# Optimization experiments

Hardware: AMD Instinct MI355X
Metric: run time of the kernel (lower is better)

The kernel has to match this reference:

```python
import jax, jax.numpy as jnp
import numpy as np

T, B, D, H, L = 512, 64, 512, 512, 2  # seq_len, batch, input, hidden, layers (bidirectional)


def _xavier(k, shape):
    fan_out, fan_in = shape
    lim = np.sqrt(6.0 / (fan_in + fan_out)).astype(np.float32)
    return jax.random.uniform(k, shape, minval=-lim, maxval=lim, dtype=jnp.float32)


def setup_inputs() -> dict:
    key = jax.random.key(0)
    ks = jax.random.split(key, 1 + 4 * L)
    inp = {"x": jax.random.normal(ks[0], (T, B, D), dtype=jnp.float32)}
    idx = 1
    for layer in range(L):
        din = D if layer == 0 else 2 * H
        for d in ("f", "b"):
            inp[f"w_ih{layer}_{d}"] = _xavier(ks[idx], (4 * H, din)); idx += 1
            inp[f"w_hh{layer}_{d}"] = _xavier(ks[idx], (4 * H, H)); idx += 1
            # xavier_uniform() in the module fills both biases with forget_bias=1.0
            inp[f"b_ih{layer}_{d}"] = jnp.ones((4 * H,), jnp.float32)
            inp[f"b_hh{layer}_{d}"] = jnp.ones((4 * H,), jnp.float32)
    return inp


def _lstm_dir(x, w_ih, w_hh, b_ih, b_hh, reverse):
    """Run one direction of a VarLSTMCell over time. x: [T,B,Din] -> h: [T,B,H]."""
    hdim = w_hh.shape[1]
    # precompute input contribution for all timesteps (same math as per-step matmul)
    xg = jnp.einsum('tbd,gd->tbg', x, w_ih) + b_ih + b_hh  # [T,B,4H]

    def step(carry, xg_t):
        h, c = carry
        gates = xg_t + h @ w_hh.T  # [B,4H]
        i, f, g, o = jnp.split(gates, 4, axis=-1)  # PyTorch LSTMCell gate order
        c = jax.nn.sigmoid(f) * c + jax.nn.sigmoid(i) * jnp.tanh(g)
        h = jax.nn.sigmoid(o) * jnp.tanh(c)
        return (h, c), h

    init = (jnp.zeros((x.shape[1], hdim), x.dtype), jnp.zeros((x.shape[1], hdim), x.dtype))
    _, hs = jax.lax.scan(step, init, xg, reverse=reverse)
    return hs  # [T,B,H], time-ordered (scan reverse keeps original ordering)


def reference(x,
              w_ih0_f, w_hh0_f, b_ih0_f, b_hh0_f,
              w_ih0_b, w_hh0_b, b_ih0_b, b_hh0_b,
              w_ih1_f, w_hh1_f, b_ih1_f, b_hh1_f,
              w_ih1_b, w_hh1_b, b_ih1_b, b_hh1_b):
    params = [
        ((w_ih0_f, w_hh0_f, b_ih0_f, b_hh0_f), (w_ih0_b, w_hh0_b, b_ih0_b, b_hh0_b)),
        ((w_ih1_f, w_hh1_f, b_ih1_f, b_hh1_f), (w_ih1_b, w_hh1_b, b_ih1_b, b_hh1_b)),
    ]
    out = x
    for fwd_p, bwd_p in params:
        h_f = _lstm_dir(out, *fwd_p, reverse=False)
        h_b = _lstm_dir(out, *bwd_p, reverse=True)
        out = jnp.concatenate([h_f, h_b], axis=-1)  # [T,B,2H]
        # dropout=0.0 -> inter-layer dropout is identity
    return out
```

## Files before the change

### kernel.cpp

```cpp
#include <hip/hip_runtime.h>
#include <hip/hip_bf16.h>
#include <stdint.h>


typedef __attribute__((ext_vector_type(8))) _Float16 half8;
typedef __attribute__((ext_vector_type(4))) float f32x4;
typedef __attribute__((ext_vector_type(4))) uint32_t u32x4;
typedef unsigned long long ull;

#define AS(p, v) __hip_atomic_store((p), (v), __ATOMIC_RELAXED, __HIP_MEMORY_SCOPE_AGENT)

#define TAGMASK 0x4000400040004000ULL
#define TM32    0x40004000u
#define PAT_L1A 0x0000400000004000ULL
#define PAT_L1B 0x4000000040000000ULL
#define PAT_INIT_LO 0x40004000u
#define PAT_INIT_HI 0x00000000u

__device__ __forceinline__ unsigned short f2h(float f) {
    union { _Float16 h; unsigned short u; } c; c.h = (_Float16)f; return c.u;
}
__device__ __forceinline__ float h2f(unsigned short u) {
    union { _Float16 h; unsigned short u; } c; c.u = u; return (float)c.h;
}

__global__ __launch_bounds__(256) void prep_kernel(
    const float* __restrict__ x,
    const float* __restrict__ w0f, const float* __restrict__ w0b,
    const float* __restrict__ w1f, const float* __restrict__ w1b,
    const float* __restrict__ bi0f, const float* __restrict__ bh0f,
    const float* __restrict__ bi0b, const float* __restrict__ bh0b,
    const float* __restrict__ bi1f, const float* __restrict__ bh1f,
    const float* __restrict__ bi1b, const float* __restrict__ bh1b,
    unsigned short* __restrict__ xh,
    unsigned short* __restrict__ wihh,
    float* __restrict__ bias,
    uint32_t* __restrict__ hbufi)
{
    const long total = 5801984L;
    long stride = (long)gridDim.x * blockDim.x;
    for (long i = (long)blockIdx.x * blockDim.x + threadIdx.x; i < total; i += stride) {
        if (i < 4194304L) {
            float4 v = ((const float4*)x)[i];
            ushort4 o; o.x=f2h(v.x); o.y=f2h(v.y); o.z=f2h(v.z); o.w=f2h(v.w);
            ((ushort4*)xh)[i] = o;
        } else if (i < 5767168L) {
            long j = i - 4194304L;
            const float* src; long sq;
            if (j < 262144L)       { src = w0f; sq = j;            }
            else if (j < 524288L)  { src = w0b; sq = j - 262144L;  }
            else if (j < 1048576L) { src = w1f; sq = j - 524288L;  }
            else                   { src = w1b; sq = j - 1048576L; }
            float4 v = ((const float4*)src)[sq];
            ushort4 o; o.x=f2h(v.x); o.y=f2h(v.y); o.z=f2h(v.z); o.w=f2h(v.w);
            ((ushort4*)wihh)[j] = o;
        } else if (i < 5769216L) {
            long j = i - 5767168L;
            int ld = (int)(j >> 9);
            long cq = j & 511L;
            const float* bi = ld==0?bi0f: ld==1?bi0b: ld==2?bi1f:bi1b;
            const float* bh = ld==0?bh0f: ld==1?bh0b: ld==2?bh1f:bh1b;
            float4 a = ((const float4*)bi)[cq];
            float4 b = ((const float4*)bh)[cq];
            float4 o; o.x=a.x+b.x; o.y=a.y+b.y; o.z=a.z+b.z; o.w=a.w+b.w;
            ((float4*)bias)[ld*512 + cq] = o;
        } else {
            long j = i - 5769216L;
            uint4 p; p.x=PAT_INIT_LO; p.y=PAT_INIT_HI; p.z=PAT_INIT_LO; p.w=PAT_INIT_HI;
            ((uint4*)hbufi)[j] = p;
        }
    }
}

__global__ __launch_bounds__(256) void gemm_xg(
    const unsigned short* __restrict__ A,
    const unsigned short* __restrict__ Wf,
    const unsigned short* __restrict__ Wb,
    unsigned short* __restrict__ xg,
    int Din)
{
    __shared__ __align__(16) unsigned short As[4096];
    __shared__ __align__(16) unsigned short Bs[4096];
    const int dir = blockIdx.z;
    const unsigned short* W = dir ? Wb : Wf;
    unsigned short* out = xg + (size_t)dir * 32768 * 2048;
    const int bn = blockIdx.x, bm = blockIdx.y;
    const int tid = threadIdx.x;
    const int wave = tid >> 6, lane = tid & 63;
    const int q = lane >> 4, ln = lane & 15;
    const int wm = wave >> 1, wn = wave & 1;

    f32x4 acc[4][4];
#pragma unroll
    for (int a = 0; a < 4; ++a)
#pragma unroll
        for (int b = 0; b < 4; ++b) acc[a][b] = (f32x4){0.f, 0.f, 0.f, 0.f};

    const int kiter = Din >> 5;
    for (int kb = 0; kb < kiter; ++kb) {
        __syncthreads();
#pragma unroll
        for (int i = 0; i < 2; ++i) {
            int off = i*4096 + wave*1024 + lane*16;
            int row = off >> 6;
            int kel = (off & 63) >> 1;
            const unsigned short* sa = A + (size_t)(bm*128 + row)*Din + kb*32 + kel;
            const unsigned short* sb = W + (size_t)(bn*128 + row)*Din + kb*32 + kel;
            __builtin_amdgcn_global_load_lds(
                (const __attribute__((address_space(1))) uint32_t*)sa,
                (__attribute__((address_space(3))) uint32_t*)((char*)As + i*4096 + wave*1024),
                16, 0, 0);
            __builtin_amdgcn_global_load_lds(
                (const __attribute__((address_space(1))) uint32_t*)sb,
                (__attribute__((address_space(3))) uint32_t*)((char*)Bs + i*4096 + wave*1024),
                16, 0, 0);
        }
        __syncthreads();
        half8 af[4], bf[4];
#pragma unroll
        for (int mt = 0; mt < 4; ++mt)
            af[mt] = *(const half8*)((const char*)As + (wm*64 + mt*16 + ln)*64 + q*16);
#pragma unroll
        for (int nt = 0; nt < 4; ++nt)
            bf[nt] = *(const half8*)((const char*)Bs + (wn*64 + nt*16 + ln)*64 + q*16);
#pragma unroll
        for (int mt = 0; mt < 4; ++mt)
#pragma unroll
            for (int nt = 0; nt < 4; ++nt)
                acc[mt][nt] = __builtin_amdgcn_mfma_f32_16x16x32_f16(af[mt], bf[nt], acc[mt][nt], 0, 0, 0);
    }
    const int tt = bm*2 + wm;
#pragma unroll
    for (int mt = 0; mt < 4; ++mt)
#pragma unroll
        for (int nt = 0; nt < 4; ++nt) {
            int col = bn*128 + wn*64 + nt*16 + ln;
            int gate = col >> 9, colg = col & 511;
            union { unsigned short u[4]; ull v; } p;
#pragma unroll
            for (int r = 0; r < 4; ++r) p.u[r] = f2h(acc[mt][nt][r]);
            __builtin_nontemporal_store(p.v,
                (ull*)(out + (((size_t)tt*4 + gate)*512 + colg)*64 + mt*16 + q*4));
        }
}

__global__ __launch_bounds__(512, 2) void rec_kernel(
    const unsigned short* __restrict__ xg,
    const float* __restrict__ whhf,
    const float* __restrict__ whhb,
    const float* __restrict__ bias,
    unsigned short* __restrict__ hbuf,
    unsigned short* __restrict__ outh,
    float* __restrict__ outf,
    const int layer)
{
    __shared__ __align__(16) unsigned short h_lds[8192];
    __shared__ __align__(16) float accbuf[2048];
    __shared__ __align__(16) unsigned short htile[512];

    const int bx = blockIdx.x;
    const int dir = bx & 1, bh = (bx >> 1) & 3, cg = bx >> 3;
    const int R0 = bh * 16, C0 = cg * 32;
    const int tid = threadIdx.x;
    const int wv = tid >> 6, lane = tid & 63;
    const int g = wv >> 1, wc = wv & 1;
    const int ln = lane & 15, q = lane >> 4;
    const float* whhg = dir ? whhb : whhf;

    const ull pat0 = layer ? PAT_L1A : 0ULL;
    const ull pat1 = layer ? PAT_L1B : TAGMASK;
    const uint32_t ep0 = (uint32_t)(pat0 & 0xffffffffULL);
    const uint32_t ep1 = (uint32_t)(pat1 & 0xffffffffULL);

    half8 wreg[16];
    {
        const int wrow = g*512 + C0 + wc*16 + ln;
        const float* wsrc = whhg + (size_t)wrow * 512 + q*8;
#pragma unroll
        for (int kk = 0; kk < 16; ++kk) {
            float4 v0 = *(const float4*)(wsrc + kk*32);
            float4 v1 = *(const float4*)(wsrc + kk*32 + 4);
            union { unsigned short u[8]; half8 v; } p;
            p.u[0]=f2h(v0.x); p.u[1]=f2h(v0.y); p.u[2]=f2h(v0.z); p.u[3]=f2h(v0.w);
            p.u[4]=f2h(v1.x); p.u[5]=f2h(v1.y); p.u[6]=f2h(v1.z); p.u[7]=f2h(v1.w);
            wreg[kk] = p.v;
        }
    }

    const unsigned short* xgd = xg + (size_t)dir * 32768 * 2048;
    const float* biasd = bias + dir * 2048;
    const int myc = C0 + wc*16 + ln;
    float bv0 = biasd[0*512 + myc];
    float bv1 = biasd[1*512 + myc];
    float bv2 = biasd[2*512 + myc];
    float bv3 = biasd[3*512 + myc];
    float carr[4] = {0.f, 0.f, 0.f, 0.f};

    const int prow = tid >> 5;
    const int pcol = (tid & 31) * 16;
    const int swz  = (prow & 7) << 4;
    const int wb0 = prow*1024 + ((pcol*2)      ^ swz);
    const int wb1 = prow*1024 + ((pcol*2 + 16) ^ swz);

#pragma unroll 1
    for (int s = 0; s < 512; ++s) {
        const int t = dir ? (511 - s) : s;

        ull xv64[4] = {0,0,0,0};
        if (g == 0) {
#pragma unroll
            for (int nt_ = 0; nt_ < 4; ++nt_)
                xv64[nt_] = __builtin_nontemporal_load(
                    (const ull*)(xgd + ((size_t)(t*4 + nt_)*512 + myc)*64 + bh*16 + q*4));
        }

        if (s > 0) {
            const int slot_r = (s - 1) & 3;
            const uint32_t ep = (((s - 1) >> 2) & 1) ? ep1 : ep0;
            const uint32_t* src = (const uint32_t*)(hbuf
                + ((size_t)(slot_r*2 + dir)*64 + R0 + prow)*512 + pcol);
            u32x4 r0, r1;
            bool ok = false;
            for (int it = 0; it < (1 << 13) && !ok; ++it) {
                asm volatile(
                    "global_load_dwordx4 %0, %2, off sc0 sc1\n\t"
                    "global_load_dwordx4 %1, %3, off sc0 sc1\n\t"
                    "s_waitcnt vmcnt(0)"
                    : "=&v"(r0), "=&v"(r1)
                    : "v"(src), "v"(src + 4)
                    : "memory");
                uint32_t bad = 0;
#pragma unroll
                for (int c = 0; c < 4; ++c) bad |= (r0[c] ^ ep) & TM32;
#pragma unroll
                for (int c = 0; c < 4; ++c) bad |= (r1[c] ^ ep) & TM32;
                ok = (bad == 0);
            }
#pragma unroll
            for (int c = 0; c < 4; ++c) { r0[c] &= ~TM32; r1[c] &= ~TM32; }
            *(u32x4*)((char*)h_lds + wb0) = r0;
            *(u32x4*)((char*)h_lds + wb1) = r1;
        }
        __syncthreads();

        f32x4 acc = (f32x4){0.f, 0.f, 0.f, 0.f};
        if (s > 0) {
            const char* hbase = (const char*)h_lds + ln*1024;
            const int lswz = (ln & 7) << 4;
#pragma unroll
            for (int kk = 0; kk < 16; ++kk) {
                half8 a = *(const half8*)(hbase + ((kk*64 + q*16) ^ lswz));
                acc = __builtin_amdgcn_mfma_f32_16x16x32_f16(a, wreg[kk], acc, 0, 0, 0);
            }
        }
        *(f32x4*)&accbuf[(wv*16 + ln)*16 + q*4] = acc;
        __syncthreads();

        if (g == 0) {
            f32x4 a0 = *(const f32x4*)&accbuf[((0*2 + wc)*16 + ln)*16 + q*4];
            f32x4 a1 = *(const f32x4*)&accbuf[((1*2 + wc)*16 + ln)*16 + q*4];
            f32x4 a2 = *(const f32x4*)&accbuf[((2*2 + wc)*16 + ln)*16 + q*4];
            f32x4 a3 = *(const f32x4*)&accbuf[((3*2 + wc)*16 + ln)*16 + q*4];
            unsigned short hs[4];
#pragma unroll
            for (int r = 0; r < 4; ++r) {
                float gi = a0[r] + h2f((unsigned short)(xv64[0] >> (16*r))) + bv0;
                float gf = a1[r] + h2f((unsigned short)(xv64[1] >> (16*r))) + bv1;
                float gg = a2[r] + h2f((unsigned short)(xv64[2] >> (16*r))) + bv2;
                float go = a3[r] + h2f((unsigned short)(xv64[3] >> (16*r))) + bv3;
                float si = 1.f / (1.f + __expf(-gi));
                float sf = 1.f / (1.f + __expf(-gf));
                float so = 1.f / (1.f + __expf(-go));
                float tg = 2.f / (1.f + __expf(-2.f*gg)) - 1.f;
                float c  = sf * carr[r] + si * tg;
                carr[r] = c;
                float th = 2.f / (1.f + __expf(-2.f*c)) - 1.f;
                hs[r] = f2h(so * th);
            }
            unsigned short* ht = htile + wc*256;
#pragma unroll
            for (int r = 0; r < 4; ++r) ht[(q*4 + r)*16 + ln] = hs[r];
            ull hv64 = *(const ull*)(ht + (lane >> 2)*16 + (lane & 3)*4);
            const int row  = R0 + (lane >> 2);
            const int colw = C0 + wc*16 + (lane & 3)*4;

            const int slot_w = s & 3;
            const ull wpat = ((s >> 2) & 1) ? pat1 : pat0;
            AS((ull*)(hbuf + ((size_t)(slot_w*2 + dir)*64 + row)*512 + colw), hv64 | wpat);

            if (layer == 0) {
                __builtin_nontemporal_store(hv64,
                    (ull*)(outh + ((size_t)t*64 + row)*1024 + dir*512 + colw));
            } else {
                union { ull u; unsigned short us[4]; } pu; pu.u = hv64;
                union { ull u; float f[2]; } o0, o1;
                o0.f[0] = h2f(pu.us[0]); o0.f[1] = h2f(pu.us[1]);
                o1.f[0] = h2f(pu.us[2]); o1.f[1] = h2f(pu.us[3]);
                ull* dst = (ull*)(outf + ((size_t)t*64 + row)*1024 + dir*512 + colw);
                __builtin_nontemporal_store(o0.u, dst);
                __builtin_nontemporal_store(o1.u, dst + 1);
            }
        }
    }
}

extern "C" void kernel_launch(void* const* d_in, const int* in_sizes, int n_in,
                              void* d_out, int out_size, void* d_ws, size_t ws_size,
                              hipStream_t stream)
{
    (void)in_sizes; (void)n_in; (void)out_size; (void)ws_size;
    const float* x       = (const float*)d_in[0];
    const float* w_ih0_f = (const float*)d_in[1];
    const float* w_hh0_f = (const float*)d_in[2];
    const float* b_ih0_f = (const float*)d_in[3];
    const float* b_hh0_f = (const float*)d_in[4];
    const float* w_ih0_b = (const float*)d_in[5];
    const float* w_hh0_b = (const float*)d_in[6];
    const float* b_ih0_b = (const float*)d_in[7];
    const float* b_hh0_b = (const float*)d_in[8];
    const float* w_ih1_f = (const float*)d_in[9];
    const float* w_hh1_f = (const float*)d_in[10];
    const float* b_ih1_f = (const float*)d_in[11];
    const float* b_hh1_f = (const float*)d_in[12];
    const float* w_ih1_b = (const float*)d_in[13];
    const float* w_hh1_b = (const float*)d_in[14];
    const float* b_ih1_b = (const float*)d_in[15];
    const float* b_hh1_b = (const float*)d_in[16];

    char* ws = (char*)d_ws;
    unsigned short* xg    = (unsigned short*)(ws + 0);
    unsigned short* wihh  = (unsigned short*)(ws + 268435456L);
    float*          bias  = (float*)         (ws + 281018368L);
    unsigned short* hbuf  = (unsigned short*)(ws + 281051136L);

    unsigned short* in1 = (unsigned short*)d_out;
    unsigned short* xh  = (unsigned short*)((char*)d_out + 67108864L);
    float* outf = (float*)d_out;

    prep_kernel<<<dim3(1024), dim3(256), 0, stream>>>(
        x, w_ih0_f, w_ih0_b, w_ih1_f, w_ih1_b,
        b_ih0_f, b_hh0_f, b_ih0_b, b_hh0_b,
        b_ih1_f, b_hh1_f, b_ih1_b, b_hh1_b,
        xh, wihh, bias, (uint32_t*)hbuf);

    gemm_xg<<<dim3(16, 256, 2), dim3(256), 0, stream>>>(
        xh, wihh, wihh + 1048576, xg, 512);
    rec_kernel<<<dim3(128), dim3(512), 0, stream>>>(
        xg, w_hh0_f, w_hh0_b, bias, hbuf, in1, (float*)nullptr, 0);

    gemm_xg<<<dim3(16, 256, 2), dim3(256), 0, stream>>>(
        in1, wihh + 2097152, wihh + 4194304, xg, 1024);
    rec_kernel<<<dim3(128), dim3(512), 0, stream>>>(
        xg, w_hh1_f, w_hh1_b, bias + 4096, hbuf,
        (unsigned short*)nullptr, outf, 1);
}
```

Measured before the change: 5.589 ms.

## Interleave forward and backward directions in one block of the recurrent kernel

Each recurrent block now handles both directions for its tile, alternating forward and backward half-steps, with double-buffered LDS and both weight sets held in registers. The grid is halved from 128 to 64 blocks. The aim is to hide cross-block flag-poll latency for one direction behind the other direction's compute, and to prefetch the next step's input gates a step ahead. In exchange it doubles register pressure for weights and serialises two directions per block, which may reduce parallelism and occupancy.

```diff
diff --git a/kernel.cpp b/kernel.cpp
--- a/kernel.cpp
+++ b/kernel.cpp
@@ -144,6 +144,112 @@
         }
 }
 
+struct RecCtx {
+    const unsigned short* hbuf_c;
+    unsigned short* hbuf;
+    unsigned short* outh;
+    float* outf;
+    int layer, R0, C0, tid, wv, lane, g, wc, ln, q;
+    int c0row, colq, wb0, wb1;
+    uint32_t ep0, ep1;
+    ull pat0, pat1;
+};
+
+__device__ __forceinline__ void poll_stage(const RecCtx& cx, int d, int sm1,
+                                           unsigned short* lbuf)
+{
+    const int slot_r = sm1 & 3;
+    const uint32_t ep = ((sm1 >> 2) & 1) ? cx.ep1 : cx.ep0;
+    const uint32_t* s0 = (const uint32_t*)(cx.hbuf_c
+        + ((size_t)(slot_r*2 + d)*64 + cx.R0 + cx.c0row)*512 + cx.colq);
+    const uint32_t* s1 = (const uint32_t*)(cx.hbuf_c
+        + ((size_t)(slot_r*2 + d)*64 + cx.R0 + cx.c0row + 8)*512 + cx.colq);
+    u32x4 r0, r1;
+    bool ok = false;
+    for (int it = 0; it < (1 << 13) && !ok; ++it) {
+        asm volatile(
+            "global_load_dwordx4 %0, %2, off sc0 sc1\n\t"
+            "global_load_dwordx4 %1, %3, off sc0 sc1\n\t"
+            "s_waitcnt vmcnt(0)"
+            : "=&v"(r0), "=&v"(r1)
+            : "v"(s0), "v"(s1)
+            : "memory");
+        uint32_t bad = 0;
+#pragma unroll
+        for (int c = 0; c < 4; ++c) bad |= (r0[c] ^ ep) & TM32;
+#pragma unroll
+        for (int c = 0; c < 4; ++c) bad |= (r1[c] ^ ep) & TM32;
+        ok = (bad == 0);
+    }
+#pragma unroll
+    for (int c = 0; c < 4; ++c) { r0[c] &= ~TM32; r1[c] &= ~TM32; }
+    *(u32x4*)((char*)lbuf + cx.wb0) = r0;
+    *(u32x4*)((char*)lbuf + cx.wb1) = r1;
+}
+
+__device__ __forceinline__ void mfma_phase(const RecCtx& cx,
+    const unsigned short* lbuf, const half8* wreg, float* achb)
+{
+    f32x4 acc = (f32x4){0.f, 0.f, 0.f, 0.f};
+    const char* hbase = (const char*)lbuf + cx.ln*1024;
+    const int lswz = (cx.ln & 7) << 4;
+#pragma unroll
+    for (int kk = 0; kk < 16; ++kk) {
+        half8 a = *(const half8*)(hbase + ((kk*64 + cx.q*16) ^ lswz));
+        acc = __builtin_amdgcn_mfma_f32_16x16x32_f16(a, wreg[kk], acc, 0, 0, 0);
+    }
+    *(f32x4*)&achb[(cx.wv*16 + cx.ln)*20 + cx.q*4] = acc;
+}
+
+__device__ __forceinline__ void pointwise(const RecCtx& cx, int d, int s, int t,
+    const ull* xv, float* carr, const float* achb, unsigned short* htb,
+    float bv0, float bv1, float bv2, float bv3)
+{
+    f32x4 a0 = *(const f32x4*)&achb[((0*2 + cx.wc)*16 + cx.ln)*20 + cx.q*4];
+    f32x4 a1 = *(const f32x4*)&achb[((1*2 + cx.wc)*16 + cx.ln)*20 + cx.q*4];
+    f32x4 a2 = *(const f32x4*)&achb[((2*2 + cx.wc)*16 + cx.ln)*20 + cx.q*4];
+    f32x4 a3 = *(const f32x4*)&achb[((3*2 + cx.wc)*16 + cx.ln)*20 + cx.q*4];
+    unsigned short hs[4];
+#pragma unroll
+    for (int r = 0; r < 4; ++r) {
+        float gi = a0[r] + h2f((unsigned short)(xv[0] >> (16*r))) + bv0;
+        float gf = a1[r] + h2f((unsigned short)(xv[1] >> (16*r))) + bv1;
+        float gg = a2[r] + h2f((unsigned short)(xv[2] >> (16*r))) + bv2;
+        float go = a3[r] + h2f((unsigned short)(xv[3] >> (16*r))) + bv3;
+        float si = 1.f / (1.f + __expf(-gi));
+        float sf = 1.f / (1.f + __expf(-gf));
+        float so = 1.f / (1.f + __expf(-go));
+        float tg = 2.f / (1.f + __expf(-2.f*gg)) - 1.f;
+        float c  = sf * carr[r] + si * tg;
+        carr[r] = c;
+        float th = 2.f / (1.f + __expf(-2.f*c)) - 1.f;
+        hs[r] = f2h(so * th);
+    }
+    unsigned short* ht = htb + cx.wc*256;
+#pragma unroll
+    for (int r = 0; r < 4; ++r) ht[(cx.q*4 + r)*16 + cx.ln] = hs[r];
+    ull hv64 = *(const ull*)(ht + (cx.lane >> 2)*16 + (cx.lane & 3)*4);
+    const int row  = cx.R0 + (cx.lane >> 2);
+    const int colw = cx.C0 + cx.wc*16 + (cx.lane & 3)*4;
+
+    const int slot_w = s & 3;
+    const ull wpat = ((s >> 2) & 1) ? cx.pat1 : cx.pat0;
+    AS((ull*)(cx.hbuf + ((size_t)(slot_w*2 + d)*64 + row)*512 + colw), hv64 | wpat);
+
+    if (cx.layer == 0) {
+        __builtin_nontemporal_store(hv64,
+            (ull*)(cx.outh + ((size_t)t*64 + row)*1024 + d*512 + colw));
+    } else {
+        union { ull u; unsigned short us[4]; } pu; pu.u = hv64;
+        union { ull u; float f[2]; } o0, o1;
+        o0.f[0] = h2f(pu.us[0]); o0.f[1] = h2f(pu.us[1]);
+        o1.f[0] = h2f(pu.us[2]); o1.f[1] = h2f(pu.us[3]);
+        ull* dst = (ull*)(cx.outf + ((size_t)t*64 + row)*1024 + d*512 + colw);
+        __builtin_nontemporal_store(o0.u, dst);
+        __builtin_nontemporal_store(o1.u, dst + 1);
+    }
+}
+
 __global__ __launch_bounds__(512, 2) void rec_kernel(
     const unsigned short* __restrict__ xg,
     const float* __restrict__ whhf,
@@ -154,152 +260,120 @@
     float* __restrict__ outf,
     const int layer)
 {
-    __shared__ __align__(16) unsigned short h_lds[8192];
-    __shared__ __align__(16) float accbuf[2048];
-    __shared__ __align__(16) unsigned short htile[512];
+    __shared__ __align__(16) unsigned short h_lds[2][8192];
+    __shared__ __align__(16) float accbuf[2][2560];
+    __shared__ __align__(16) unsigned short htile[2][512];
 
     const int bx = blockIdx.x;
-    const int dir = bx & 1, bh = (bx >> 1) & 3, cg = bx >> 3;
-    const int R0 = bh * 16, C0 = cg * 32;
-    const int tid = threadIdx.x;
-    const int wv = tid >> 6, lane = tid & 63;
-    const int g = wv >> 1, wc = wv & 1;
-    const int ln = lane & 15, q = lane >> 4;
-    const float* whhg = dir ? whhb : whhf;
-
-    const ull pat0 = layer ? PAT_L1A : 0ULL;
-    const ull pat1 = layer ? PAT_L1B : TAGMASK;
-    const uint32_t ep0 = (uint32_t)(pat0 & 0xffffffffULL);
-    const uint32_t ep1 = (uint32_t)(pat1 & 0xffffffffULL);
-
-    half8 wreg[16];
+    RecCtx cx;
+    cx.hbuf_c = hbuf; cx.hbuf = hbuf; cx.outh = outh; cx.outf = outf;
+    cx.layer = layer;
+    const int bh = bx & 3, cg = bx >> 2;
+    cx.R0 = bh * 16; cx.C0 = cg * 32;
+    cx.tid = threadIdx.x;
+    cx.wv = cx.tid >> 6; cx.lane = cx.tid & 63;
+    cx.g = cx.wv >> 1; cx.wc = cx.wv & 1;
+    cx.ln = cx.lane & 15; cx.q = cx.lane >> 4;
+    cx.pat0 = layer ? PAT_L1A : 0ULL;
+    cx.pat1 = layer ? PAT_L1B : TAGMASK;
+    cx.ep0 = (uint32_t)(cx.pat0 & 0xffffffffULL);
+    cx.ep1 = (uint32_t)(cx.pat1 & 0xffffffffULL);
+    cx.c0row = cx.tid >> 6;
+    cx.colq  = (cx.tid & 63) * 8;
+    cx.wb0 = cx.c0row*1024 + (((cx.tid & 63)*16) ^ ((cx.c0row & 7) << 4));
+    cx.wb1 = (cx.c0row + 8)*1024 + (((cx.tid & 63)*16) ^ ((cx.c0row & 7) << 4));
+
+    half8 wregA[16], wregB[16];
     {
-        const int wrow = g*512 + C0 + wc*16 + ln;
-        const float* wsrc = whhg + (size_t)wrow * 512 + q*8;
+        const int wrow = cx.g*512 + cx.C0 + cx.wc*16 + cx.ln;
+        const float* srcA = whhf + (size_t)wrow * 512 + cx.q*8;
+        const float* srcB = whhb + (size_t)wrow * 512 + cx.q*8;
 #pragma unroll
         for (int kk = 0; kk < 16; ++kk) {
-            float4 v0 = *(const float4*)(wsrc + kk*32);
-            float4 v1 = *(const float4*)(wsrc + kk*32 + 4);
+            float4 v0 = *(const float4*)(srcA + kk*32);
+            float4 v1 = *(const float4*)(srcA + kk*32 + 4);
             union { unsigned short u[8]; half8 v; } p;
             p.u[0]=f2h(v0.x); p.u[1]=f2h(v0.y); p.u[2]=f2h(v0.z); p.u[3]=f2h(v0.w);
             p.u[4]=f2h(v1.x); p.u[5]=f2h(v1.y); p.u[6]=f2h(v1.z); p.u[7]=f2h(v1.w);
-            wreg[kk] = p.v;
-        }
-    }
-
-    const unsigned short* xgd = xg + (size_t)dir * 32768 * 2048;
-    const float* biasd = bias + dir * 2048;
-    const int myc = C0 + wc*16 + ln;
-    float bv0 = biasd[0*512 + myc];
-    float bv1 = biasd[1*512 + myc];
-    float bv2 = biasd[2*512 + myc];
-    float bv3 = biasd[3*512 + myc];
-    float carr[4] = {0.f, 0.f, 0.f, 0.f};
-
-    const int prow = tid >> 5;
-    const int pcol = (tid & 31) * 16;
-    const int swz  = (prow & 7) << 4;
-    const int wb0 = prow*1024 + ((pcol*2)      ^ swz);
-    const int wb1 = prow*1024 + ((pcol*2 + 16) ^ swz);
+            wregA[kk] = p.v;
+        }
+#pragma unroll
+        for (int kk = 0; kk < 16; ++kk) {
+            float4 v0 = *(const float4*)(srcB + kk*32);
+            float4 v1 = *(const float4*)(srcB + kk*32 + 4);
+            union { unsigned short u[8]; half8 v; } p;
+            p.u[0]=f2h(v0.x); p.u[1]=f2h(v0.y); p.u[2]=f2h(v0.z); p.u[3]=f2h(v0.w);
+            p.u[4]=f2h(v1.x); p.u[5]=f2h(v1.y); p.u[6]=f2h(v1.z); p.u[7]=f2h(v1.w);
+            wregB[kk] = p.v;
+        }
+    }
+
+    const unsigned short* xgdA = xg;
+    const unsigned short* xgdB = xg + (size_t)32768 * 2048;
+    const int myc = cx.C0 + cx.wc*16 + cx.ln;
+    float bvA0 = bias[0*512 + myc],        bvA1 = bias[1*512 + myc];
+    float bvA2 = bias[2*512 + myc],        bvA3 = bias[3*512 + myc];
+    float bvB0 = bias[2048 + 0*512 + myc], bvB1 = bias[2048 + 1*512 + myc];
+    float bvB2 = bias[2048 + 2*512 + myc], bvB3 = bias[2048 + 3*512 + myc];
+    float carrA[4] = {0.f,0.f,0.f,0.f}, carrB[4] = {0.f,0.f,0.f,0.f};
+    ull xvA[4] = {0,0,0,0}, xvB[4] = {0,0,0,0};
+    ull xvAn[4] = {0,0,0,0}, xvBn[4] = {0,0,0,0};
+
+    const size_t xoff = (size_t)bh*16 + cx.q*4;
+
+    {
+        f32x4 z = (f32x4){0.f,0.f,0.f,0.f};
+        *(f32x4*)&accbuf[0][(cx.wv*16 + cx.ln)*20 + cx.q*4] = z;
+        *(f32x4*)&accbuf[1][(cx.wv*16 + cx.ln)*20 + cx.q*4] = z;
+        __syncthreads();
+        if (cx.g == 0) {
+#pragma unroll
+            for (int k = 0; k < 4; ++k) {
+                xvA[k] = __builtin_nontemporal_load(
+                    (const ull*)(xgdA + ((size_t)(0*4 + k)*512 + myc)*64 + xoff));
+                xvB[k] = __builtin_nontemporal_load(
+                    (const ull*)(xgdB + ((size_t)(511*4 + k)*512 + myc)*64 + xoff));
+            }
+            pointwise(cx, 0, 0, 0,   xvA, carrA, accbuf[0], htile[0], bvA0,bvA1,bvA2,bvA3);
+            pointwise(cx, 1, 0, 511, xvB, carrB, accbuf[1], htile[1], bvB0,bvB1,bvB2,bvB3);
+#pragma unroll
+            for (int k = 0; k < 4; ++k) {
+                xvA[k] = __builtin_nontemporal_load(
+                    (const ull*)(xgdA + ((size_t)(1*4 + k)*512 + myc)*64 + xoff));
+                xvB[k] = __builtin_nontemporal_load(
+                    (const ull*)(xgdB + ((size_t)(510*4 + k)*512 + myc)*64 + xoff));
+            }
+        }
+    }
 
 #pragma unroll 1
-    for (int s = 0; s < 512; ++s) {
-        const int t = dir ? (511 - s) : s;
-
-        ull xv64[4] = {0,0,0,0};
-        if (g == 0) {
-#pragma unroll
-            for (int nt_ = 0; nt_ < 4; ++nt_)
-                xv64[nt_] = __builtin_nontemporal_load(
-                    (const ull*)(xgd + ((size_t)(t*4 + nt_)*512 + myc)*64 + bh*16 + q*4));
-        }
-
-        if (s > 0) {
-            const int slot_r = (s - 1) & 3;
-            const uint32_t ep = (((s - 1) >> 2) & 1) ? ep1 : ep0;
-            const uint32_t* src = (const uint32_t*)(hbuf
-                + ((size_t)(slot_r*2 + dir)*64 + R0 + prow)*512 + pcol);
-            u32x4 r0, r1;
-            bool ok = false;
-            for (int it = 0; it < (1 << 13) && !ok; ++it) {
-                asm volatile(
-                    "global_load_dwordx4 %0, %2, off sc0 sc1\n\t"
-                    "global_load_dwordx4 %1, %3, off sc0 sc1\n\t"
-                    "s_waitcnt vmcnt(0)"
-                    : "=&v"(r0), "=&v"(r1)
-                    : "v"(src), "v"(src + 4)
-                    : "memory");
-                uint32_t bad = 0;
-#pragma unroll
-                for (int c = 0; c < 4; ++c) bad |= (r0[c] ^ ep) & TM32;
-#pragma unroll
-                for (int c = 0; c < 4; ++c) bad |= (r1[c] ^ ep) & TM32;
-                ok = (bad == 0);
+    for (int s = 1; s < 512; ++s) {
+        const int tA = s, tB = 511 - s;
+
+        poll_stage(cx, 0, s - 1, h_lds[0]);
+        __syncthreads();
+        if (cx.g == 0 && s < 511) {
+#pragma unroll
+            for (int k = 0; k < 4; ++k) {
+                xvAn[k] = __builtin_nontemporal_load(
+                    (const ull*)(xgdA + ((size_t)((s+1)*4 + k)*512 + myc)*64 + xoff));
+                xvBn[k] = __builtin_nontemporal_load(
+                    (const ull*)(xgdB + ((size_t)((510-s)*4 + k)*512 + myc)*64 + xoff));
             }
-#pragma unroll
-            for (int c = 0; c < 4; ++c) { r0[c] &= ~TM32; r1[c] &= ~TM32; }
-            *(u32x4*)((char*)h_lds + wb0) = r0;
-            *(u32x4*)((char*)h_lds + wb1) = r1;
-        }
-        __syncthreads();
-
-        f32x4 acc = (f32x4){0.f, 0.f, 0.f, 0.f};
-        if (s > 0) {
-            const char* hbase = (const char*)h_lds + ln*1024;
-            const int lswz = (ln & 7) << 4;
-#pragma unroll
-            for (int kk = 0; kk < 16; ++kk) {
-                half8 a = *(const half8*)(hbase + ((kk*64 + q*16) ^ lswz));
-                acc = __builtin_amdgcn_mfma_f32_16x16x32_f16(a, wreg[kk], acc, 0, 0, 0);
-            }
-        }
-        *(f32x4*)&accbuf[(wv*16 + ln)*16 + q*4] = acc;
-        __syncthreads();
-
-        if (g == 0) {
-            f32x4 a0 = *(const f32x4*)&accbuf[((0*2 + wc)*16 + ln)*16 + q*4];
-            f32x4 a1 = *(const f32x4*)&accbuf[((1*2 + wc)*16 + ln)*16 + q*4];
-            f32x4 a2 = *(const f32x4*)&accbuf[((2*2 + wc)*16 + ln)*16 + q*4];
-            f32x4 a3 = *(const f32x4*)&accbuf[((3*2 + wc)*16 + ln)*16 + q*4];
-            unsigned short hs[4];
-#pragma unroll
-            for (int r = 0; r < 4; ++r) {
-                float gi = a0[r] + h2f((unsigned short)(xv64[0] >> (16*r))) + bv0;
-                float gf = a1[r] + h2f((unsigned short)(xv64[1] >> (16*r))) + bv1;
-                float gg = a2[r] + h2f((unsigned short)(xv64[2] >> (16*r))) + bv2;
-                float go = a3[r] + h2f((unsigned short)(xv64[3] >> (16*r))) + bv3;
-                float si = 1.f / (1.f + __expf(-gi));
-                float sf = 1.f / (1.f + __expf(-gf));
-                float so = 1.f / (1.f + __expf(-go));
-                float tg = 2.f / (1.f + __expf(-2.f*gg)) - 1.f;
-                float c  = sf * carr[r] + si * tg;
-                carr[r] = c;
-                float th = 2.f / (1.f + __expf(-2.f*c)) - 1.f;
-                hs[r] = f2h(so * th);
-            }
-            unsigned short* ht = htile + wc*256;
-#pragma unroll
-            for (int r = 0; r < 4; ++r) ht[(q*4 + r)*16 + ln] = hs[r];
-            ull hv64 = *(const ull*)(ht + (lane >> 2)*16 + (lane & 3)*4);
-            const int row  = R0 + (lane >> 2);
-            const int colw = C0 + wc*16 + (lane & 3)*4;
-
-            const int slot_w = s & 3;
-            const ull wpat = ((s >> 2) & 1) ? pat1 : pat0;
-            AS((ull*)(hbuf + ((size_t)(slot_w*2 + dir)*64 + row)*512 + colw), hv64 | wpat);
-
-            if (layer == 0) {
-                __builtin_nontemporal_store(hv64,
-                    (ull*)(outh + ((size_t)t*64 + row)*1024 + dir*512 + colw));
-            } else {
-                union { ull u; unsigned short us[4]; } pu; pu.u = hv64;
-                union { ull u; float f[2]; } o0, o1;
-                o0.f[0] = h2f(pu.us[0]); o0.f[1] = h2f(pu.us[1]);
-                o1.f[0] = h2f(pu.us[2]); o1.f[1] = h2f(pu.us[3]);
-                ull* dst = (ull*)(outf + ((size_t)t*64 + row)*1024 + dir*512 + colw);
-                __builtin_nontemporal_store(o0.u, dst);
-                __builtin_nontemporal_store(o1.u, dst + 1);
-            }
+        }
+        mfma_phase(cx, h_lds[0], wregA, accbuf[0]);
+        __syncthreads();
+        if (cx.g == 0)
+            pointwise(cx, 0, s, tA, xvA, carrA, accbuf[0], htile[0], bvA0,bvA1,bvA2,bvA3);
+
+        poll_stage(cx, 1, s - 1, h_lds[1]);
+        __syncthreads();
+        mfma_phase(cx, h_lds[1], wregB, accbuf[1]);
+        __syncthreads();
+        if (cx.g == 0) {
+            pointwise(cx, 1, s, tB, xvB, carrB, accbuf[1], htile[1], bvB0,bvB1,bvB2,bvB3);
+#pragma unroll
+            for (int k = 0; k < 4; ++k) { xvA[k] = xvAn[k]; xvB[k] = xvBn[k]; }
         }
     }
 }
@@ -345,12 +419,12 @@
 
     gemm_xg<<<dim3(16, 256, 2), dim3(256), 0, stream>>>(
         xh, wihh, wihh + 1048576, xg, 512);
-    rec_kernel<<<dim3(128), dim3(512), 0, stream>>>(
+    rec_kernel<<<dim3(64), dim3(512), 0, stream>>>(
         xg, w_hh0_f, w_hh0_b, bias, hbuf, in1, (float*)nullptr, 0);
 
     gemm_xg<<<dim3(16, 256, 2), dim3(256), 0, stream>>>(
         in1, wihh + 2097152, wihh + 4194304, xg, 1024);
-    rec_kernel<<<dim3(128), dim3(512), 0, stream>>>(
+    rec_kernel<<<dim3(64), dim3(512), 0, stream>>>(
         xg, w_hh1_f, w_hh1_b, bias + 4096, hbuf,
         (unsigned short*)nullptr, outf, 1);
 }
```

New measurement: 5.106 ms. 1.09x faster.

## Interleave both LSTM directions per block with pipelined hidden-state loads

Applied to the files above, without the earlier changes.

Each recurrent block now handles both the forward and backward directions for its row and column tile, keeping both recurrent weight sets in registers and halving the grid to 64 blocks. The hidden-state ring reads for one direction are issued while the other direction does its MFMA and pointwise work, so polling latency overlaps with compute. Gates are laid out so one wave holds all four gates of a column and combines them with lane shuffles, which drops the shared-memory accumulator exchange and one barrier. Register pressure doubles (launch bounds drop to one block per CU) and each step is now serialized over two directions within a block.

```diff
diff --git a/kernel.cpp b/kernel.cpp
--- a/kernel.cpp
+++ b/kernel.cpp
@@ -144,7 +144,7 @@
         }
 }
 
-__global__ __launch_bounds__(512, 2) void rec_kernel(
+__global__ __launch_bounds__(512, 1) void rec_kernel(
     const unsigned short* __restrict__ xg,
     const float* __restrict__ whhf,
     const float* __restrict__ whhb,
@@ -154,153 +154,199 @@
     float* __restrict__ outf,
     const int layer)
 {
-    __shared__ __align__(16) unsigned short h_lds[8192];
-    __shared__ __align__(16) float accbuf[2048];
+    __shared__ __align__(16) unsigned short h_lds[32768];
     __shared__ __align__(16) unsigned short htile[512];
 
     const int bx = blockIdx.x;
-    const int dir = bx & 1, bh = (bx >> 1) & 3, cg = bx >> 3;
-    const int R0 = bh * 16, C0 = cg * 32;
+    const int bh = bx & 3, cg = bx >> 2;
+    const int R0 = bh*16, C0 = cg*32;
     const int tid = threadIdx.x;
     const int wv = tid >> 6, lane = tid & 63;
-    const int g = wv >> 1, wc = wv & 1;
     const int ln = lane & 15, q = lane >> 4;
-    const float* whhg = dir ? whhb : whhf;
+    const int gate = ln & 3, lc = ln >> 2;
+    const int col = C0 + wv*4 + lc;
 
     const ull pat0 = layer ? PAT_L1A : 0ULL;
     const ull pat1 = layer ? PAT_L1B : TAGMASK;
     const uint32_t ep0 = (uint32_t)(pat0 & 0xffffffffULL);
     const uint32_t ep1 = (uint32_t)(pat1 & 0xffffffffULL);
-
-    half8 wreg[16];
+    const uint32_t NC = layer ? 0u : 0x40000000u;
+
+    half8 wregA[16], wregB[16];
     {
-        const int wrow = g*512 + C0 + wc*16 + ln;
-        const float* wsrc = whhg + (size_t)wrow * 512 + q*8;
+        const float* srcA = whhf + (size_t)(gate*512 + col)*512 + q*8;
+        const float* srcB = whhb + (size_t)(gate*512 + col)*512 + q*8;
 #pragma unroll
         for (int kk = 0; kk < 16; ++kk) {
-            float4 v0 = *(const float4*)(wsrc + kk*32);
-            float4 v1 = *(const float4*)(wsrc + kk*32 + 4);
+            float4 v0 = *(const float4*)(srcA + kk*32);
+            float4 v1 = *(const float4*)(srcA + kk*32 + 4);
             union { unsigned short u[8]; half8 v; } p;
             p.u[0]=f2h(v0.x); p.u[1]=f2h(v0.y); p.u[2]=f2h(v0.z); p.u[3]=f2h(v0.w);
             p.u[4]=f2h(v1.x); p.u[5]=f2h(v1.y); p.u[6]=f2h(v1.z); p.u[7]=f2h(v1.w);
-            wreg[kk] = p.v;
+            wregA[kk] = p.v;
+        }
+#pragma unroll
+        for (int kk = 0; kk < 16; ++kk) {
+            float4 v0 = *(const float4*)(srcB + kk*32);
+            float4 v1 = *(const float4*)(srcB + kk*32 + 4);
+            union { unsigned short u[8]; half8 v; } p;
+            p.u[0]=f2h(v0.x); p.u[1]=f2h(v0.y); p.u[2]=f2h(v0.z); p.u[3]=f2h(v0.w);
+            p.u[4]=f2h(v1.x); p.u[5]=f2h(v1.y); p.u[6]=f2h(v1.z); p.u[7]=f2h(v1.w);
+            wregB[kk] = p.v;
         }
     }
 
-    const unsigned short* xgd = xg + (size_t)dir * 32768 * 2048;
-    const float* biasd = bias + dir * 2048;
-    const int myc = C0 + wc*16 + ln;
-    float bv0 = biasd[0*512 + myc];
-    float bv1 = biasd[1*512 + myc];
-    float bv2 = biasd[2*512 + myc];
-    float bv3 = biasd[3*512 + myc];
-    float carr[4] = {0.f, 0.f, 0.f, 0.f};
-
-    const int prow = tid >> 5;
-    const int pcol = (tid & 31) * 16;
-    const int swz  = (prow & 7) << 4;
-    const int wb0 = prow*1024 + ((pcol*2)      ^ swz);
-    const int wb1 = prow*1024 + ((pcol*2 + 16) ^ swz);
-
-#pragma unroll 1
-    for (int s = 0; s < 512; ++s) {
-        const int t = dir ? (511 - s) : s;
-
-        ull xv64[4] = {0,0,0,0};
-        if (g == 0) {
-#pragma unroll
-            for (int nt_ = 0; nt_ < 4; ++nt_)
-                xv64[nt_] = __builtin_nontemporal_load(
-                    (const ull*)(xgd + ((size_t)(t*4 + nt_)*512 + myc)*64 + bh*16 + q*4));
-        }
-
-        if (s > 0) {
-            const int slot_r = (s - 1) & 3;
-            const uint32_t ep = (((s - 1) >> 2) & 1) ? ep1 : ep0;
-            const uint32_t* src = (const uint32_t*)(hbuf
-                + ((size_t)(slot_r*2 + dir)*64 + R0 + prow)*512 + pcol);
-            u32x4 r0, r1;
-            bool ok = false;
-            for (int it = 0; it < (1 << 13) && !ok; ++it) {
-                asm volatile(
-                    "global_load_dwordx4 %0, %2, off sc0 sc1\n\t"
-                    "global_load_dwordx4 %1, %3, off sc0 sc1\n\t"
-                    "s_waitcnt vmcnt(0)"
-                    : "=&v"(r0), "=&v"(r1)
-                    : "v"(src), "v"(src + 4)
-                    : "memory");
-                uint32_t bad = 0;
-#pragma unroll
-                for (int c = 0; c < 4; ++c) bad |= (r0[c] ^ ep) & TM32;
-#pragma unroll
-                for (int c = 0; c < 4; ++c) bad |= (r1[c] ^ ep) & TM32;
-                ok = (bad == 0);
+    const int c0row = tid >> 6;
+    const int colq  = (tid & 63) * 8;
+    const int swz   = (c0row & 7) << 4;
+    const int wb0 = c0row*1024 + (((tid & 63)*16) ^ swz);
+    const int wb1 = (c0row + 8)*1024 + (((tid & 63)*16) ^ swz);
+
+    const unsigned short* xgdA = xg;
+    const unsigned short* xgdB = xg + (size_t)32768 * 2048;
+    const float bvA = bias[gate*512 + col];
+    const float bvB = bias[2048 + gate*512 + col];
+    float carrA[4] = {0.f,0.f,0.f,0.f}, carrB[4] = {0.f,0.f,0.f,0.f};
+
+    auto xga = [&](int t) { return (const ull*)(xgdA + ((size_t)(t*4 + gate)*512 + col)*64 + bh*16 + q*4); };
+    auto xgb = [&](int t) { return (const ull*)(xgdB + ((size_t)(t*4 + gate)*512 + col)*64 + bh*16 + q*4); };
+    auto ringaddr = [&](int d, int sm1) {
+        return (const uint32_t*)(hbuf + ((size_t)((sm1 & 3)*2 + d)*64 + R0 + c0row)*512 + colq);
+    };
+
+    auto TAGS = [&](const u32x4& r0, const u32x4& r1, uint32_t ep) -> uint32_t {
+        uint32_t bad = 0;
+#pragma unroll
+        for (int c = 0; c < 4; ++c) bad |= (r0[c] ^ ep) & TM32;
+#pragma unroll
+        for (int c = 0; c < 4; ++c) bad |= (r1[c] ^ ep) & TM32;
+        return bad;
+    };
+    auto ISSUE = [&](u32x4& r0, u32x4& r1, const uint32_t* a0) {
+        r0 = (u32x4){NC, NC, NC, NC};
+        r1 = (u32x4){NC, NC, NC, NC};
+        asm volatile("global_load_dwordx4 %0, %2, off sc0 sc1\n\t"
+                     "global_load_dwordx4 %1, %3, off sc0 sc1"
+                     : "+v"(r0), "+v"(r1)
+                     : "v"(a0), "v"(a0 + 2048) : "memory");
+    };
+    auto CHECKSTAGE = [&](u32x4& r0, u32x4& r1, const uint32_t* a0, uint32_t ep,
+                          unsigned short* lbuf, int N) {
+        if (N == 2) asm volatile("s_waitcnt vmcnt(2)" : "+v"(r0), "+v"(r1) :: "memory");
+        else        asm volatile("s_waitcnt vmcnt(4)" : "+v"(r0), "+v"(r1) :: "memory");
+        uint32_t bad = TAGS(r0, r1, ep);
+        if (__builtin_expect(bad != 0, 0)) {
+            asm volatile("s_waitcnt vmcnt(0)" : "+v"(r0), "+v"(r1) :: "memory");
+            bad = TAGS(r0, r1, ep);
+            for (int it = 0; bad && it < (1 << 13); ++it) {
+                asm volatile("global_load_dwordx4 %0, %2, off sc0 sc1\n\t"
+                             "global_load_dwordx4 %1, %3, off sc0 sc1\n\t"
+                             "s_waitcnt vmcnt(0)"
+                             : "+v"(r0), "+v"(r1)
+                             : "v"(a0), "v"(a0 + 2048) : "memory");
+                bad = TAGS(r0, r1, ep);
             }
-#pragma unroll
-            for (int c = 0; c < 4; ++c) { r0[c] &= ~TM32; r1[c] &= ~TM32; }
-            *(u32x4*)((char*)h_lds + wb0) = r0;
-            *(u32x4*)((char*)h_lds + wb1) = r1;
-        }
-        __syncthreads();
-
-        f32x4 acc = (f32x4){0.f, 0.f, 0.f, 0.f};
-        if (s > 0) {
-            const char* hbase = (const char*)h_lds + ln*1024;
-            const int lswz = (ln & 7) << 4;
-#pragma unroll
-            for (int kk = 0; kk < 16; ++kk) {
-                half8 a = *(const half8*)(hbase + ((kk*64 + q*16) ^ lswz));
-                acc = __builtin_amdgcn_mfma_f32_16x16x32_f16(a, wreg[kk], acc, 0, 0, 0);
-            }
-        }
-        *(f32x4*)&accbuf[(wv*16 + ln)*16 + q*4] = acc;
-        __syncthreads();
-
-        if (g == 0) {
-            f32x4 a0 = *(const f32x4*)&accbuf[((0*2 + wc)*16 + ln)*16 + q*4];
-            f32x4 a1 = *(const f32x4*)&accbuf[((1*2 + wc)*16 + ln)*16 + q*4];
-            f32x4 a2 = *(const f32x4*)&accbuf[((2*2 + wc)*16 + ln)*16 + q*4];
-            f32x4 a3 = *(const f32x4*)&accbuf[((3*2 + wc)*16 + ln)*16 + q*4];
-            unsigned short hs[4];
-#pragma unroll
-            for (int r = 0; r < 4; ++r) {
-                float gi = a0[r] + h2f((unsigned short)(xv64[0] >> (16*r))) + bv0;
-                float gf = a1[r] + h2f((unsigned short)(xv64[1] >> (16*r))) + bv1;
-                float gg = a2[r] + h2f((unsigned short)(xv64[2] >> (16*r))) + bv2;
-                float go = a3[r] + h2f((unsigned short)(xv64[3] >> (16*r))) + bv3;
-                float si = 1.f / (1.f + __expf(-gi));
-                float sf = 1.f / (1.f + __expf(-gf));
-                float so = 1.f / (1.f + __expf(-go));
-                float tg = 2.f / (1.f + __expf(-2.f*gg)) - 1.f;
-                float c  = sf * carr[r] + si * tg;
-                carr[r] = c;
-                float th = 2.f / (1.f + __expf(-2.f*c)) - 1.f;
-                hs[r] = f2h(so * th);
-            }
-            unsigned short* ht = htile + wc*256;
-#pragma unroll
-            for (int r = 0; r < 4; ++r) ht[(q*4 + r)*16 + ln] = hs[r];
-            ull hv64 = *(const ull*)(ht + (lane >> 2)*16 + (lane & 3)*4);
-            const int row  = R0 + (lane >> 2);
-            const int colw = C0 + wc*16 + (lane & 3)*4;
-
-            const int slot_w = s & 3;
+        }
+        u32x4 w0 = r0, w1 = r1;
+#pragma unroll
+        for (int c = 0; c < 4; ++c) { w0[c] &= ~TM32; w1[c] &= ~TM32; }
+        *(u32x4*)((char*)lbuf + wb0) = w0;
+        *(u32x4*)((char*)lbuf + wb1) = w1;
+    };
+    auto MFMA = [&](const unsigned short* lbuf, const half8* wreg) -> f32x4 {
+        f32x4 acc = (f32x4){0.f,0.f,0.f,0.f};
+        const char* hb = (const char*)lbuf + ln*1024;
+        const int lswz = (ln & 7) << 4;
+#pragma unroll
+        for (int kk = 0; kk < 16; ++kk) {
+            half8 a = *(const half8*)(hb + ((kk*64 + q*16) ^ lswz));
+            acc = __builtin_amdgcn_mfma_f32_16x16x32_f16(a, wreg[kk], acc, 0, 0, 0);
+        }
+        return acc;
+    };
+    auto PW = [&](int d, int s, int t, f32x4 acc, ull xv, float* carr, float bv) {
+        unsigned short hs[4];
+#pragma unroll
+        for (int r = 0; r < 4; ++r) {
+            float v  = acc[r] + h2f((unsigned short)(xv >> (16*r))) + bv;
+            float o1 = __shfl_xor(v, 1);
+            float e  = (gate & 1) ? o1 : v;
+            float od = (gate & 1) ? v  : o1;
+            float e2 = __shfl_xor(e, 2);
+            float od2= __shfl_xor(od, 2);
+            float gi = (gate & 2) ? e2 : e;
+            float gg = (gate & 2) ? e  : e2;
+            float gf = (gate & 2) ? od2: od;
+            float go = (gate & 2) ? od : od2;
+            float si = 1.f / (1.f + __expf(-gi));
+            float sf = 1.f / (1.f + __expf(-gf));
+            float so = 1.f / (1.f + __expf(-go));
+            float tg = 2.f / (1.f + __expf(-2.f*gg)) - 1.f;
+            float c  = sf * carr[r] + si * tg;
+            carr[r] = c;
+            float th = 2.f / (1.f + __expf(-2.f*c)) - 1.f;
+            hs[r] = f2h(so * th);
+        }
+        if (gate == 0) {
+#pragma unroll
+            for (int r = 0; r < 4; ++r) htile[wv*64 + (q*4 + r)*4 + lc] = hs[r];
+        }
+        if (lane < 16) {
+            ull hv64 = *(const ull*)(htile + wv*64 + lane*4);
+            const int row  = R0 + lane;
+            const int colb = C0 + wv*4;
             const ull wpat = ((s >> 2) & 1) ? pat1 : pat0;
-            AS((ull*)(hbuf + ((size_t)(slot_w*2 + dir)*64 + row)*512 + colw), hv64 | wpat);
-
+            AS((ull*)(hbuf + ((size_t)((s & 3)*2 + d)*64 + row)*512 + colb), hv64 | wpat);
             if (layer == 0) {
                 __builtin_nontemporal_store(hv64,
-                    (ull*)(outh + ((size_t)t*64 + row)*1024 + dir*512 + colw));
+                    (ull*)(outh + ((size_t)t*64 + row)*1024 + d*512 + colb));
             } else {
                 union { ull u; unsigned short us[4]; } pu; pu.u = hv64;
-                union { ull u; float f[2]; } o0, o1;
-                o0.f[0] = h2f(pu.us[0]); o0.f[1] = h2f(pu.us[1]);
-                o1.f[0] = h2f(pu.us[2]); o1.f[1] = h2f(pu.us[3]);
-                ull* dst = (ull*)(outf + ((size_t)t*64 + row)*1024 + dir*512 + colw);
-                __builtin_nontemporal_store(o0.u, dst);
-                __builtin_nontemporal_store(o1.u, dst + 1);
+                f32x4 o; o[0]=h2f(pu.us[0]); o[1]=h2f(pu.us[1]);
+                o[2]=h2f(pu.us[2]); o[3]=h2f(pu.us[3]);
+                __builtin_nontemporal_store(o,
+                    (f32x4*)(outf + ((size_t)t*64 + row)*1024 + d*512 + colb));
             }
         }
+    };
+
+    u32x4 rA0, rA1, rB0, rB1;
+    ull xvA, xvB, xvAn, xvBn;
+
+    {
+        f32x4 z = (f32x4){0.f,0.f,0.f,0.f};
+        xvA = __builtin_nontemporal_load(xga(0));
+        xvB = __builtin_nontemporal_load(xgb(511));
+        PW(0, 0, 0,   z, xvA, carrA, bvA);
+        PW(1, 0, 511, z, xvB, carrB, bvB);
+        xvA = __builtin_nontemporal_load(xga(1));
+        xvB = __builtin_nontemporal_load(xgb(510));
+        ISSUE(rA0, rA1, ringaddr(0, 0));
+    }
+
+#pragma unroll 1
+    for (int s = 1; s < 512; ++s) {
+        const int tA = s, tB = 511 - s;
+        unsigned short* bufA = h_lds + ((s & 1)) * 8192;
+        unsigned short* bufB = h_lds + (2 + (s & 1)) * 8192;
+        const uint32_t ep = (((s - 1) >> 2) & 1) ? ep1 : ep0;
+
+        CHECKSTAGE(rA0, rA1, ringaddr(0, s - 1), ep, bufA, 2);
+        ISSUE(rB0, rB1, ringaddr(1, s - 1));
+        __syncthreads();
+        f32x4 accA = MFMA(bufA, wregA);
+        if (s < 511) {
+            xvAn = __builtin_nontemporal_load(xga(s + 1));
+            xvBn = __builtin_nontemporal_load(xgb(510 - s));
+        }
+        PW(0, s, tA, accA, xvA, carrA, bvA);
+
+        CHECKSTAGE(rB0, rB1, ringaddr(1, s - 1), ep, bufB, 4);
+        ISSUE(rA0, rA1, ringaddr(0, s));
+        __syncthreads();
+        f32x4 accB = MFMA(bufB, wregB);
+        PW(1, s, tB, accB, xvB, carrB, bvB);
+        xvA = xvAn; xvB = xvBn;
     }
 }
 
@@ -345,12 +391,12 @@
 
     gemm_xg<<<dim3(16, 256, 2), dim3(256), 0, stream>>>(
         xh, wihh, wihh + 1048576, xg, 512);
-    rec_kernel<<<dim3(128), dim3(512), 0, stream>>>(
+    rec_kernel<<<dim3(64), dim3(512), 0, stream>>>(
         xg, w_hh0_f, w_hh0_b, bias, hbuf, in1, (float*)nullptr, 0);
 
     gemm_xg<<<dim3(16, 256, 2), dim3(256), 0, stream>>>(
         in1, wihh + 2097152, wihh + 4194304, xg, 1024);
-    rec_kernel<<<dim3(128), dim3(512), 0, stream>>>(
+    rec_kernel<<<dim3(64), dim3(512), 0, stream>>>(
         xg, w_hh1_f, w_hh1_b, bias + 4096, hbuf,
         (unsigned short*)nullptr, outf, 1);
 }
```

Result: slower. 7.158 ms (+28.1%).
